# Performance work log

Measured on AMD Instinct MI355X. Metric: run time of the kernel, lower is better.

The kernel has to match this reference:

```python
import jax, jax.numpy as jnp
import numpy as np
import math

NUM_HEADS = 8
RES_K = 9  # res_kernel_size


def setup_inputs() -> dict:
    key = jax.random.key(0)
    ks = jax.random.split(key, 6)
    N, C, h, w = 8, 256, 64, 64
    x = jax.random.normal(ks[0], (N, C, h, w), dtype=jnp.float32)
    w_qkv = jax.random.normal(ks[1], (3 * C, C), dtype=jnp.float32) * 0.02
    b_qkv = jax.random.normal(ks[2], (3 * C,), dtype=jnp.float32) * 0.02
    w_proj = jax.random.normal(ks[3], (C, C), dtype=jnp.float32) * 0.02
    b_proj = jax.random.normal(ks[4], (C,), dtype=jnp.float32) * 0.02
    w_dconv = jax.random.normal(ks[5], (NUM_HEADS, 1, RES_K, 1), dtype=jnp.float32) * 0.1
    return {"x": x, "w_qkv": w_qkv, "b_qkv": b_qkv,
            "w_proj": w_proj, "b_proj": b_proj, "w_dconv": w_dconv}


def _l2norm(t):
    # torch x / x.norm(dim=-1, keepdim=True): plain L2 norm, no eps
    return t / jnp.linalg.norm(t, axis=-1, keepdims=True)


def reference(x, w_qkv, b_qkv, w_proj, b_proj, w_dconv):
    N, C, h, w = x.shape
    H = NUM_HEADS
    D = C // H
    L = h * w
    xt = x.reshape(N, C, L).transpose(0, 2, 1)  # [N, L, C]
    qkv = xt @ w_qkv.T + b_qkv                   # [N, L, 3C]
    qkv = qkv.reshape(N, L, 3, H, D).transpose(2, 0, 3, 1, 4)  # [3, N, H, L, D]
    q, k, v = qkv[0], qkv[1], qkv[2]
    q = _l2norm(q)
    k = _l2norm(k)
    # depthwise conv over token dim: v as NCHW with C=H, H=L, W=D
    pad = RES_K // 2
    dconv_v = jax.lax.conv_general_dilated(
        v, w_dconv, window_strides=(1, 1), padding=[(pad, pad), (0, 0)],
        dimension_numbers=("NCHW", "OIHW", "NCHW"), feature_group_count=H)
    attn = jnp.einsum("nhld,nhle->nhde", k, v)   # [N, H, D, D]
    out = 0.5 * v + (1.0 / math.pi) * jnp.einsum("nhld,nhde->nhle", q, attn)
    out = _l2norm(out)
    out = out + dconv_v
    out = out.transpose(0, 2, 1, 3).reshape(N, L, C)  # [N, L, C]
    out = out @ w_proj.T + b_proj
    return out.transpose(0, 2, 1).reshape(N, C, h, w)
```

## Files before the change

### kernel.cpp

```cpp
#include <hip/hip_runtime.h>

#define NB 8
#define CC 256
#define HH 8
#define DD 32
#define LL 4096

typedef short v8s __attribute__((ext_vector_type(8)));
typedef float v4f __attribute__((ext_vector_type(4)));
typedef unsigned short v8u __attribute__((ext_vector_type(8)));
typedef unsigned short v4us __attribute__((ext_vector_type(4)));

__device__ __forceinline__ float4 ld4(const float* p) { return *(const float4*)p; }

__device__ __forceinline__ unsigned short f2bf(float f) {
    union { float f; unsigned int u; } v; v.f = f;
    unsigned int r = (v.u + 0x7FFFu + ((v.u >> 16) & 1u)) >> 16;
    return (unsigned short)r;
}
__device__ __forceinline__ float bf2f(unsigned short u) {
    union { unsigned int u; float f; } v; v.u = ((unsigned int)u) << 16;
    return v.f;
}

__device__ __forceinline__ void gl_lds16(const unsigned short* g, unsigned short* l) {
    __builtin_amdgcn_global_load_lds(
        (const __attribute__((address_space(1))) void*)g,
        (__attribute__((address_space(3))) void*)l, 16, 0, 0);
}

__global__ __launch_bounds__(256) void cvt2_k(
    const float* __restrict__ a, const float* __restrict__ b,
    unsigned short* __restrict__ da, unsigned short* __restrict__ db,
    int na, int nb)
{
    int i = blockIdx.x * 256 + threadIdx.x;
    if (i < na) da[i] = f2bf(a[i]);
    else if (i - na < nb) db[i - na] = f2bf(b[i - na]);
}

#define PADC 264
__global__ __launch_bounds__(256) void transpose_x_k(
    const float* __restrict__ x, unsigned short* __restrict__ xb)
{
    __shared__ unsigned short t[32][PADC];
    const int n = blockIdx.y;
    const int l0 = blockIdx.x * 32;
    const float* xn = x + (size_t)n * CC * LL;
    const int lam = threadIdx.x & 31;
    const int cb = threadIdx.x >> 5;
#pragma unroll
    for (int i = 0; i < 32; ++i) {
        int c = cb * 32 + i;
        t[lam][c] = f2bf(xn[(size_t)c * LL + l0 + lam]);
    }
    __syncthreads();
    unsigned short* dst = xb + ((size_t)n * LL + l0) * CC;
    const int tid = threadIdx.x;
#pragma unroll
    for (int i = 0; i < 4; ++i) {
        int f = i * 2048 + tid * 8;
        int lr = f >> 8;
        int c2 = f & 255;
        v8u val = *(const v8u*)&t[lr][c2];
        *(v8u*)(dst + f) = val;
    }
}

__global__ __launch_bounds__(256, 2) void gemm_qkv_mfma(
    const unsigned short* __restrict__ xb, const unsigned short* __restrict__ wqb,
    const float* __restrict__ bqkv,
    unsigned short* __restrict__ q, unsigned short* __restrict__ k,
    unsigned short* __restrict__ v)
{
    __shared__ __align__(16) unsigned short xs[8192];
    __shared__ __align__(16) unsigned short wsb[8192];

    const int bid  = blockIdx.x;
    const int xcd  = bid & 7;
    const int slot = bid >> 3;
    const int jt   = slot % 6;
    const int p    = slot / 6;
    const int gp   = xcd * 32 + p;
    const int l0   = (gp & 31) * 128;
    const int n    = gp >> 5;
    const int j0   = jt * 128;

    const int tid = threadIdx.x;
    const int lane = tid & 63, wave = tid >> 6;
    const int wr = wave >> 1, wc = wave & 1;
    const int r = lane & 15, quad = lane >> 4;

    const int srow = wave * 8 + (lane >> 3);
    const int dchunk = (lane & 7) ^ (lane >> 3);
    const unsigned short* xg = xb + (size_t)n * LL * CC
                             + (size_t)(l0 + srow) * CC + dchunk * 8;
    const unsigned short* wg = wqb + (size_t)(j0 + srow) * CC + dchunk * 8;
    unsigned short* xls = xs + wave * 512 + lane * 8;
    unsigned short* wls = wsb + wave * 512 + lane * 8;

    v4f acc[4][4];
#pragma unroll
    for (int mi = 0; mi < 4; ++mi)
#pragma unroll
        for (int nj = 0; nj < 4; ++nj) acc[mi][nj] = (v4f)(0.f);

    const int jbase = wr * 64;
    const int lbase = wc * 64;

    for (int kt = 0; kt < 4; ++kt) {
        if (kt) __syncthreads();
        const int c0 = kt * 64;
#pragma unroll
        for (int i = 0; i < 4; ++i) {
            gl_lds16(xg + (size_t)i * 32 * CC + c0, xls + i * 2048);
            gl_lds16(wg + (size_t)i * 32 * CC + c0, wls + i * 2048);
        }
        __syncthreads();

        v8s a[4][2], b[4][2];
#pragma unroll
        for (int kk = 0; kk < 2; ++kk) {
            const int cfrag = kk * 4 + quad;
#pragma unroll
            for (int mi = 0; mi < 4; ++mi) {
                int jloc = jbase + mi * 16 + r;
                int s = cfrag ^ (r & 7);
                a[mi][kk] = *(const v8s*)(wsb + jloc * 64 + s * 8);
            }
#pragma unroll
            for (int nj = 0; nj < 4; ++nj) {
                int lloc = lbase + nj * 16 + r;
                int s = cfrag ^ (r & 7);
                b[nj][kk] = *(const v8s*)(xs + lloc * 64 + s * 8);
            }
        }
#pragma unroll
        for (int kk = 0; kk < 2; ++kk)
#pragma unroll
            for (int mi = 0; mi < 4; ++mi)
#pragma unroll
                for (int nj = 0; nj < 4; ++nj)
                    acc[mi][nj] = __builtin_amdgcn_mfma_f32_16x16x32_bf16(
                        a[mi][kk], b[nj][kk], acc[mi][nj], 0, 0, 0);
    }

    const int s = jt >> 1;
    unsigned short* base = (s == 0 ? q : (s == 1 ? k : v));

    float bias[4][4];
#pragma unroll
    for (int mi = 0; mi < 4; ++mi)
        *(float4*)bias[mi] = *(const float4*)(bqkv + j0 + jbase + mi * 16 + quad * 4);

    unsigned short* dstp[4];
#pragma unroll
    for (int mi = 0; mi < 4; ++mi) {
        int hh = (jt & 1) * 4 + wr * 2 + (mi >> 1);
        int d0 = (mi & 1) * 16 + quad * 4;
        dstp[mi] = base + (size_t)(n * HH + hh) * LL * DD + d0;
    }

    if (s < 2) {
#pragma unroll
        for (int nj = 0; nj < 4; ++nj) {
            float t[4][4];
            float ss[2] = {0.f, 0.f};
#pragma unroll
            for (int mi = 0; mi < 4; ++mi)
#pragma unroll
                for (int reg = 0; reg < 4; ++reg) {
                    float val = acc[mi][nj][reg] + bias[mi][reg];
                    t[mi][reg] = val;
                    ss[mi >> 1] += val * val;
                }
#pragma unroll
            for (int h2 = 0; h2 < 2; ++h2) {
                ss[h2] += __shfl_xor(ss[h2], 16);
                ss[h2] += __shfl_xor(ss[h2], 32);
                ss[h2] = rsqrtf(ss[h2]);
            }
            size_t l = (size_t)(l0 + lbase + nj * 16 + r);
#pragma unroll
            for (int mi = 0; mi < 4; ++mi) {
                float rn = ss[mi >> 1];
                v4us pk;
#pragma unroll
                for (int reg = 0; reg < 4; ++reg) pk[reg] = f2bf(t[mi][reg] * rn);
                *(v4us*)(dstp[mi] + l * DD) = pk;
            }
        }
    } else {
#pragma unroll
        for (int nj = 0; nj < 4; ++nj) {
            size_t l = (size_t)(l0 + lbase + nj * 16 + r);
#pragma unroll
            for (int mi = 0; mi < 4; ++mi) {
                v4us pk;
#pragma unroll
                for (int reg = 0; reg < 4; ++reg)
                    pk[reg] = f2bf(acc[mi][nj][reg] + bias[mi][reg]);
                *(v4us*)(dstp[mi] + l * DD) = pk;
            }
        }
    }
}

__global__ __launch_bounds__(256) void attn_k(
    const unsigned short* __restrict__ k, const unsigned short* __restrict__ v,
    float* __restrict__ attn)
{
    __shared__ float red[4][1024];
    const int nh = blockIdx.y;
    const int wv = threadIdx.x >> 6;
    const int lane = threadIdx.x & 63;
    const int eg = lane & 7;
    const int dg = lane >> 3;
    const int l0 = blockIdx.x * 512 + wv * 128;
    const unsigned short* kb = k + (size_t)nh * LL * DD;
    const unsigned short* vb = v + (size_t)nh * LL * DD;
    float acc[4][4] = {};
#pragma unroll 4
    for (int l = l0; l < l0 + 128; ++l) {
        v4us k4 = *(const v4us*)(kb + (size_t)l * DD + dg * 4);
        v4us v4 = *(const v4us*)(vb + (size_t)l * DD + eg * 4);
        float ka[4] = {bf2f(k4[0]), bf2f(k4[1]), bf2f(k4[2]), bf2f(k4[3])};
        float va[4] = {bf2f(v4[0]), bf2f(v4[1]), bf2f(v4[2]), bf2f(v4[3])};
#pragma unroll
        for (int dp = 0; dp < 4; ++dp)
#pragma unroll
            for (int ep = 0; ep < 4; ++ep)
                acc[dp][ep] += ka[dp] * va[ep];
    }
#pragma unroll
    for (int dp = 0; dp < 4; ++dp)
#pragma unroll
        for (int ep = 0; ep < 4; ++ep)
            red[wv][(dg * 4 + dp) * 32 + eg * 4 + ep] = acc[dp][ep];
    __syncthreads();
    float* ap = attn + (size_t)nh * 1024;
    for (int i = threadIdx.x; i < 1024; i += 256)
        atomicAdd(&ap[i], red[0][i] + red[1][i] + red[2][i] + red[3][i]);
}

#define TOK 256
__global__ __launch_bounds__(256) void mid_k(
    const unsigned short* __restrict__ q, const unsigned short* __restrict__ v,
    const float* __restrict__ attn, const float* __restrict__ wd,
    unsigned short* __restrict__ midb)
{
    __shared__ float vt[TOK + 8][34];
    const int nh = blockIdx.y;
    const int n = nh >> 3, hh = nh & 7;
    const int l0 = blockIdx.x * TOK;
    const int tid = threadIdx.x;
    const int lane = tid & 63, wave = tid >> 6;
    const int r = lane & 15, quad = lane >> 4;
    const unsigned short* vb = v + (size_t)nh * LL * DD;

    for (int f = tid; f < (TOK + 8) * 4; f += 256) {
        int row = f >> 2, seg = f & 3;
        int l = l0 - 4 + row;
        float tmp[8];
        if (l >= 0 && l < LL) {
            v8u v8 = *(const v8u*)(vb + (size_t)l * DD + seg * 8);
#pragma unroll
            for (int j = 0; j < 8; ++j) tmp[j] = bf2f(v8[j]);
        } else {
#pragma unroll
            for (int j = 0; j < 8; ++j) tmp[j] = 0.f;
        }
#pragma unroll
        for (int j = 0; j < 8; ++j) vt[row][seg * 8 + j] = tmp[j];
    }

    v8s bfrag[2];
#pragma unroll
    for (int et = 0; et < 2; ++et) {
        int e = et * 16 + r;
#pragma unroll
        for (int j = 0; j < 8; ++j)
            ((unsigned short*)&bfrag[et])[j] =
                f2bf(attn[(size_t)nh * 1024 + (quad * 8 + j) * 32 + e]);
    }

    float wc[9];
#pragma unroll
    for (int r9 = 0; r9 < 9; ++r9) wc[r9] = wd[hh * 9 + r9];

    __syncthreads();

    const unsigned short* qb = q + (size_t)nh * LL * DD;
    unsigned short* ob = midb + (size_t)n * LL * CC + hh * DD;

#pragma unroll
    for (int tp = 0; tp < 4; ++tp) {
        const int tb = wave * 64 + tp * 16;
        v8s afrag = *(const v8s*)(qb + (size_t)(l0 + tb + r) * DD + quad * 8);
        v4f acc[2] = {(v4f)(0.f), (v4f)(0.f)};
#pragma unroll
        for (int et = 0; et < 2; ++et)
            acc[et] = __builtin_amdgcn_mfma_f32_16x16x32_bf16(afrag, bfrag[et], acc[et], 0, 0, 0);

        float vcol[2][12];
#pragma unroll
        for (int et = 0; et < 2; ++et) {
            int e = et * 16 + r;
#pragma unroll
            for (int o = 0; o < 12; ++o)
                vcol[et][o] = vt[tb + quad * 4 + o][e];
        }

        float t[2][4], ss[4];
#pragma unroll
        for (int reg = 0; reg < 4; ++reg) {
            t[0][reg] = 0.5f * vcol[0][4 + reg] + 0.31830988618379067f * acc[0][reg];
            t[1][reg] = 0.5f * vcol[1][4 + reg] + 0.31830988618379067f * acc[1][reg];
            ss[reg] = t[0][reg] * t[0][reg] + t[1][reg] * t[1][reg];
        }
#pragma unroll
        for (int m = 1; m < 16; m <<= 1)
#pragma unroll
            for (int reg = 0; reg < 4; ++reg)
                ss[reg] += __shfl_xor(ss[reg], m);
#pragma unroll
        for (int reg = 0; reg < 4; ++reg) ss[reg] = rsqrtf(ss[reg]);

#pragma unroll
        for (int et = 0; et < 2; ++et) {
            int e = et * 16 + r;
#pragma unroll
            for (int reg = 0; reg < 4; ++reg) {
                float dv = 0.f;
#pragma unroll
                for (int r9 = 0; r9 < 9; ++r9) dv += wc[r9] * vcol[et][reg + r9];
                int l = l0 + tb + quad * 4 + reg;
                ob[(size_t)l * CC + e] = f2bf(t[et][reg] * ss[reg] + dv);
            }
        }
    }
}

__global__ __launch_bounds__(256, 2) void gemm_proj_mfma(
    const unsigned short* __restrict__ midb, const unsigned short* __restrict__ wpb,
    const float* __restrict__ bp, float* __restrict__ out)
{
    __shared__ __align__(16) unsigned short xs[8192];
    __shared__ __align__(16) unsigned short wsb[8192];

    const int bid  = blockIdx.x;
    const int xcd  = bid & 7;
    const int slot = bid >> 3;
    const int jt   = slot & 1;
    const int p    = slot >> 1;
    const int gp   = xcd * 32 + p;
    const int l0   = (gp & 31) * 128;
    const int n    = gp >> 5;
    const int j0   = jt * 128;

    const int tid = threadIdx.x;
    const int lane = tid & 63, wave = tid >> 6;
    const int wr = wave >> 1, wc = wave & 1;
    const int r = lane & 15, quad = lane >> 4;

    const int srow = wave * 8 + (lane >> 3);
    const int dchunk = (lane & 7) ^ (lane >> 3);
    const unsigned short* xg = midb + (size_t)n * LL * CC
                             + (size_t)(l0 + srow) * CC + dchunk * 8;
    const unsigned short* wg = wpb + (size_t)(j0 + srow) * CC + dchunk * 8;
    unsigned short* xls = xs + wave * 512 + lane * 8;
    unsigned short* wls = wsb + wave * 512 + lane * 8;

    v4f acc[4][4];
#pragma unroll
    for (int mi = 0; mi < 4; ++mi)
#pragma unroll
        for (int nj = 0; nj < 4; ++nj) acc[mi][nj] = (v4f)(0.f);

    const int jbase = wr * 64;
    const int lbase = wc * 64;

    for (int kt = 0; kt < 4; ++kt) {
        if (kt) __syncthreads();
        const int c0 = kt * 64;
#pragma unroll
        for (int i = 0; i < 4; ++i) {
            gl_lds16(xg + (size_t)i * 32 * CC + c0, xls + i * 2048);
            gl_lds16(wg + (size_t)i * 32 * CC + c0, wls + i * 2048);
        }
        __syncthreads();

        v8s a[4][2], b[4][2];
#pragma unroll
        for (int kk = 0; kk < 2; ++kk) {
            const int cfrag = kk * 4 + quad;
#pragma unroll
            for (int mi = 0; mi < 4; ++mi) {
                int jloc = jbase + mi * 16 + r;
                int s = cfrag ^ (r & 7);
                a[mi][kk] = *(const v8s*)(wsb + jloc * 64 + s * 8);
            }
#pragma unroll
            for (int nj = 0; nj < 4; ++nj) {
                int lloc = lbase + nj * 16 + r;
                int s = cfrag ^ (r & 7);
                b[nj][kk] = *(const v8s*)(xs + lloc * 64 + s * 8);
            }
        }
#pragma unroll
        for (int kk = 0; kk < 2; ++kk)
#pragma unroll
            for (int mi = 0; mi < 4; ++mi)
#pragma unroll
                for (int nj = 0; nj < 4; ++nj)
                    acc[mi][nj] = __builtin_amdgcn_mfma_f32_16x16x32_bf16(
                        a[mi][kk], b[nj][kk], acc[mi][nj], 0, 0, 0);
    }

#pragma unroll
    for (int mi = 0; mi < 4; ++mi)
#pragma unroll
        for (int reg = 0; reg < 4; ++reg) {
            int j = j0 + jbase + mi * 16 + quad * 4 + reg;
            float bias = bp[j];
#pragma unroll
            for (int nj = 0; nj < 4; ++nj) {
                int l = l0 + lbase + nj * 16 + r;
                out[((size_t)n * CC + j) * LL + l] = acc[mi][nj][reg] + bias;
            }
        }
}

extern "C" void kernel_launch(void* const* d_in, const int* in_sizes, int n_in,
                              void* d_out, int out_size, void* d_ws, size_t ws_size,
                              hipStream_t stream)
{
    const float* x     = (const float*)d_in[0];
    const float* wqkv  = (const float*)d_in[1];
    const float* bqkv  = (const float*)d_in[2];
    const float* wproj = (const float*)d_in[3];
    const float* bproj = (const float*)d_in[4];
    const float* wd    = (const float*)d_in[5];
    float* out = (float*)d_out;

    const size_t QKV = (size_t)NB * HH * LL * DD;
    unsigned short* q = (unsigned short*)d_ws;
    unsigned short* k = q + QKV;
    unsigned short* v = k + QKV;
    float* attn = (float*)(v + QKV);
    unsigned short* xb = (unsigned short*)(attn + (size_t)NB * HH * DD * DD);
    unsigned short* midb = xb;
    unsigned short* wqb = xb + (size_t)NB * LL * CC;
    unsigned short* wpb = wqb + 3 * CC * CC;

    hipMemsetAsync(attn, 0, (size_t)NB * HH * DD * DD * sizeof(float), stream);

    cvt2_k<<<1024, 256, 0, stream>>>(wqkv, wproj, wqb, wpb, 3 * CC * CC, CC * CC);
    transpose_x_k<<<dim3(128, 8), 256, 0, stream>>>(x, xb);
    gemm_qkv_mfma<<<1536, 256, 0, stream>>>(xb, wqb, bqkv, q, k, v);
    attn_k<<<dim3(8, 64), 256, 0, stream>>>(k, v, attn);
    mid_k<<<dim3(LL / TOK, 64), 256, 0, stream>>>(q, v, attn, wd, midb);
    gemm_proj_mfma<<<512, 256, 0, stream>>>(midb, wpb, bproj, out);
}
```

Baseline: 158.3 us.

## Widen QKV GEMM tile to 256 output columns and fold attn zeroing into cvt kernel

```diff
diff --git a/kernel.cpp b/kernel.cpp
--- a/kernel.cpp
+++ b/kernel.cpp
@@ -32,11 +32,12 @@
 __global__ __launch_bounds__(256) void cvt2_k(
     const float* __restrict__ a, const float* __restrict__ b,
     unsigned short* __restrict__ da, unsigned short* __restrict__ db,
-    int na, int nb)
+    float* __restrict__ attn)
 {
     int i = blockIdx.x * 256 + threadIdx.x;
-    if (i < na) da[i] = f2bf(a[i]);
-    else if (i - na < nb) db[i - na] = f2bf(b[i - na]);
+    if (i < 3 * CC * CC) da[i] = f2bf(a[i]);
+    else if (i < 4 * CC * CC) db[i - 3 * CC * CC] = f2bf(b[i - 3 * CC * CC]);
+    else attn[i - 4 * CC * CC] = 0.f;
 }
 
 #define PADC 264
@@ -74,17 +75,17 @@
     unsigned short* __restrict__ v)
 {
     __shared__ __align__(16) unsigned short xs[8192];
-    __shared__ __align__(16) unsigned short wsb[8192];
+    __shared__ __align__(16) unsigned short wsb[16384];
 
     const int bid  = blockIdx.x;
     const int xcd  = bid & 7;
     const int slot = bid >> 3;
-    const int jt   = slot % 6;
-    const int p    = slot / 6;
+    const int jt   = slot % 3;
+    const int p    = slot / 3;
     const int gp   = xcd * 32 + p;
     const int l0   = (gp & 31) * 128;
     const int n    = gp >> 5;
-    const int j0   = jt * 128;
+    const int j0   = jt * 256;
 
     const int tid = threadIdx.x;
     const int lane = tid & 63, wave = tid >> 6;
@@ -99,75 +100,73 @@
     unsigned short* xls = xs + wave * 512 + lane * 8;
     unsigned short* wls = wsb + wave * 512 + lane * 8;
 
-    v4f acc[4][4];
-#pragma unroll
-    for (int mi = 0; mi < 4; ++mi)
+    v4f acc[8][4];
+#pragma unroll
+    for (int mi = 0; mi < 8; ++mi)
 #pragma unroll
         for (int nj = 0; nj < 4; ++nj) acc[mi][nj] = (v4f)(0.f);
 
-    const int jbase = wr * 64;
+    const int jbase = wr * 128;
     const int lbase = wc * 64;
 
     for (int kt = 0; kt < 4; ++kt) {
         if (kt) __syncthreads();
         const int c0 = kt * 64;
 #pragma unroll
-        for (int i = 0; i < 4; ++i) {
+        for (int i = 0; i < 4; ++i)
             gl_lds16(xg + (size_t)i * 32 * CC + c0, xls + i * 2048);
+#pragma unroll
+        for (int i = 0; i < 8; ++i)
             gl_lds16(wg + (size_t)i * 32 * CC + c0, wls + i * 2048);
-        }
         __syncthreads();
 
-        v8s a[4][2], b[4][2];
 #pragma unroll
         for (int kk = 0; kk < 2; ++kk) {
             const int cfrag = kk * 4 + quad;
-#pragma unroll
-            for (int mi = 0; mi < 4; ++mi) {
-                int jloc = jbase + mi * 16 + r;
-                int s = cfrag ^ (r & 7);
-                a[mi][kk] = *(const v8s*)(wsb + jloc * 64 + s * 8);
-            }
+            const int s = cfrag ^ (r & 7);
+            v8s b[4];
 #pragma unroll
             for (int nj = 0; nj < 4; ++nj) {
                 int lloc = lbase + nj * 16 + r;
-                int s = cfrag ^ (r & 7);
-                b[nj][kk] = *(const v8s*)(xs + lloc * 64 + s * 8);
-            }
-        }
-#pragma unroll
-        for (int kk = 0; kk < 2; ++kk)
-#pragma unroll
-            for (int mi = 0; mi < 4; ++mi)
+                b[nj] = *(const v8s*)(xs + lloc * 64 + s * 8);
+            }
+            v8s a[8];
+#pragma unroll
+            for (int mi = 0; mi < 8; ++mi) {
+                int jloc = jbase + mi * 16 + r;
+                a[mi] = *(const v8s*)(wsb + jloc * 64 + s * 8);
+            }
+#pragma unroll
+            for (int mi = 0; mi < 8; ++mi)
 #pragma unroll
                 for (int nj = 0; nj < 4; ++nj)
                     acc[mi][nj] = __builtin_amdgcn_mfma_f32_16x16x32_bf16(
-                        a[mi][kk], b[nj][kk], acc[mi][nj], 0, 0, 0);
-    }
-
-    const int s = jt >> 1;
-    unsigned short* base = (s == 0 ? q : (s == 1 ? k : v));
-
-    float bias[4][4];
-#pragma unroll
-    for (int mi = 0; mi < 4; ++mi)
+                        a[mi], b[nj], acc[mi][nj], 0, 0, 0);
+        }
+    }
+
+    unsigned short* base = (jt == 0 ? q : (jt == 1 ? k : v));
+
+    float bias[8][4];
+#pragma unroll
+    for (int mi = 0; mi < 8; ++mi)
         *(float4*)bias[mi] = *(const float4*)(bqkv + j0 + jbase + mi * 16 + quad * 4);
 
-    unsigned short* dstp[4];
-#pragma unroll
-    for (int mi = 0; mi < 4; ++mi) {
-        int hh = (jt & 1) * 4 + wr * 2 + (mi >> 1);
+    unsigned short* dstp[8];
+#pragma unroll
+    for (int mi = 0; mi < 8; ++mi) {
+        int hh = wr * 4 + (mi >> 1);
         int d0 = (mi & 1) * 16 + quad * 4;
         dstp[mi] = base + (size_t)(n * HH + hh) * LL * DD + d0;
     }
 
-    if (s < 2) {
+    if (jt < 2) {
 #pragma unroll
         for (int nj = 0; nj < 4; ++nj) {
-            float t[4][4];
-            float ss[2] = {0.f, 0.f};
-#pragma unroll
-            for (int mi = 0; mi < 4; ++mi)
+            float t[8][4];
+            float ss[4] = {0.f, 0.f, 0.f, 0.f};
+#pragma unroll
+            for (int mi = 0; mi < 8; ++mi)
 #pragma unroll
                 for (int reg = 0; reg < 4; ++reg) {
                     float val = acc[mi][nj][reg] + bias[mi][reg];
@@ -175,14 +174,14 @@
                     ss[mi >> 1] += val * val;
                 }
 #pragma unroll
-            for (int h2 = 0; h2 < 2; ++h2) {
-                ss[h2] += __shfl_xor(ss[h2], 16);
-                ss[h2] += __shfl_xor(ss[h2], 32);
-                ss[h2] = rsqrtf(ss[h2]);
+            for (int h4 = 0; h4 < 4; ++h4) {
+                ss[h4] += __shfl_xor(ss[h4], 16);
+                ss[h4] += __shfl_xor(ss[h4], 32);
+                ss[h4] = rsqrtf(ss[h4]);
             }
             size_t l = (size_t)(l0 + lbase + nj * 16 + r);
 #pragma unroll
-            for (int mi = 0; mi < 4; ++mi) {
+            for (int mi = 0; mi < 8; ++mi) {
                 float rn = ss[mi >> 1];
                 v4us pk;
 #pragma unroll
@@ -195,7 +194,7 @@
         for (int nj = 0; nj < 4; ++nj) {
             size_t l = (size_t)(l0 + lbase + nj * 16 + r);
 #pragma unroll
-            for (int mi = 0; mi < 4; ++mi) {
+            for (int mi = 0; mi < 8; ++mi) {
                 v4us pk;
 #pragma unroll
                 for (int reg = 0; reg < 4; ++reg)
@@ -453,11 +452,9 @@
     unsigned short* wqb = xb + (size_t)NB * LL * CC;
     unsigned short* wpb = wqb + 3 * CC * CC;
 
-    hipMemsetAsync(attn, 0, (size_t)NB * HH * DD * DD * sizeof(float), stream);
-
-    cvt2_k<<<1024, 256, 0, stream>>>(wqkv, wproj, wqb, wpb, 3 * CC * CC, CC * CC);
+    cvt2_k<<<1280, 256, 0, stream>>>(wqkv, wproj, wqb, wpb, attn);
     transpose_x_k<<<dim3(128, 8), 256, 0, stream>>>(x, xb);
-    gemm_qkv_mfma<<<1536, 256, 0, stream>>>(xb, wqb, bqkv, q, k, v);
+    gemm_qkv_mfma<<<768, 256, 0, stream>>>(xb, wqb, bqkv, q, k, v);
     attn_k<<<dim3(8, 64), 256, 0, stream>>>(k, v, attn);
     mid_k<<<dim3(LL / TOK, 64), 256, 0, stream>>>(q, v, attn, wd, midb);
     gemm_proj_mfma<<<512, 256, 0, stream>>>(midb, wpb, bproj, out);
```

Measured after the change: 157.1 us. About the same (-0.8%).
